# Optimization experiments

Measured on AMD Instinct MI355X. Metric: run time of the kernel, lower is better.

Reference implementation:

```python
import jax, jax.numpy as jnp
import numpy as np

B, LQ, LK, D = 2, 2048, 2048, 1024
H, DK, DV = 16, 64, 64
EPS = 1e-6


def setup_inputs() -> dict:
    key = jax.random.key(0)
    ks = jax.random.split(key, 12)
    s = 1.0 / np.sqrt(D)
    return {
        "PE_states": jax.random.normal(ks[0], (B, LK, D), jnp.float32),
        "global_state": jax.random.normal(ks[1], (B, LQ, D), jnp.float32),
        "PE_statements": jax.random.normal(ks[2], (B, LK, D), jnp.float32),
        "PE_operators": jax.random.normal(ks[3], (B, LK, D), jnp.float32),
        "PE_solution_scores": jax.random.uniform(ks[4], (B, LK), jnp.float32),
        "mask": jax.random.randint(ks[5], (B, LQ, LK), 0, 2, jnp.int32),
        "w_q": jax.random.normal(ks[6], (D, H * DK), jnp.float32) * s,
        "w_k": jax.random.normal(ks[7], (D, H * DK), jnp.float32) * s,
        "w_v": jax.random.normal(ks[8], (D, H * DV), jnp.float32) * s,
        "w_fc": jax.random.normal(ks[9], (H * DV, D), jnp.float32) * s,
        "ln_gamma": jnp.ones((D,), jnp.float32),
        "ln_beta": jnp.zeros((D,), jnp.float32),
    }


def _layer_norm(x, gamma, beta):
    mu = jnp.mean(x, axis=-1, keepdims=True)
    var = jnp.mean(jnp.square(x - mu), axis=-1, keepdims=True)
    return (x - mu) * jax.lax.rsqrt(var + EPS) * gamma + beta


def reference(PE_states, global_state, PE_statements, PE_operators,
              PE_solution_scores, mask, w_q, w_k, w_v, w_fc, ln_gamma, ln_beta):
    # att_type == 'ca_sc', query_mode == 'PE', dropout == 0
    residual = global_state  # [B, LQ, D]
    q = (global_state @ w_q).reshape(B, LQ, H, DK).transpose(0, 2, 1, 3)   # bhqd
    k = (PE_states @ w_k).reshape(B, LK, H, DK).transpose(0, 2, 1, 3)      # bhkd
    v_s = (PE_statements @ w_v).reshape(B, LK, H, DV).transpose(0, 2, 1, 3)
    v_o = (PE_operators @ w_v).reshape(B, LK, H, DV).transpose(0, 2, 1, 3)

    temp = jnp.asarray(DK, jnp.float32) ** 0.5
    attn = jnp.einsum('bhqd,bhkd->bhqk', q / temp, k)  # [B,H,LQ,LK]
    # PE_solution_scores: per-key bias broadcast over heads and queries
    attn = (attn + PE_solution_scores[:, None, None, :]) / 2.0
    attn = jnp.where(mask[:, None, :, :] == 0, jnp.float32(-1e9), attn)
    attn = jax.nn.softmax(attn, axis=-1)

    def head_out(v):
        o = jnp.einsum('bhqk,bhkd->bhqd', attn, v)
        o = o.transpose(0, 2, 1, 3).reshape(B, LQ, H * DV)
        o = o @ w_fc + residual
        return _layer_norm(o, ln_gamma, ln_beta)

    statement_pred = head_out(v_s)
    operator_pred = head_out(v_o)
    return statement_pred, operator_pred
```

## Files before the change

### kernel.cpp

```cpp
#include <hip/hip_runtime.h>


typedef unsigned short u16;
typedef unsigned int   u32;
typedef unsigned long long u64;

typedef __attribute__((ext_vector_type(8))) short frag_ab;
typedef __attribute__((ext_vector_type(4))) float frag_cd;
typedef __attribute__((ext_vector_type(16))) float f32x16;
typedef __attribute__((ext_vector_type(8))) unsigned short u16x8;
typedef __attribute__((ext_vector_type(4))) unsigned short u16x4;
typedef __attribute__((ext_vector_type(2))) unsigned int u32x2;
typedef __attribute__((ext_vector_type(4))) int int4v;

__device__ __forceinline__ u16 f2bf(float f) {
    u32 x = __builtin_bit_cast(u32, f);
    return (u16)((x + 0x7fffu + ((x >> 16) & 1u)) >> 16);
}

__device__ __forceinline__ u32 pkbf(float a, float b) {
    return __builtin_amdgcn_perm(__builtin_bit_cast(u32, b),
                                 __builtin_bit_cast(u32, a), 0x07060302u);
}

#define GLDS16(gsrc, ldst)                                                     \
    __builtin_amdgcn_global_load_lds(                                          \
        (const __attribute__((address_space(1))) void*)(gsrc),                 \
        (__attribute__((address_space(3))) void*)(ldst), 16, 0, 0)

#define MFMA32(a, b, c) __builtin_amdgcn_mfma_f32_32x32x16_bf16(a, b, c, 0, 0, 0)

__global__ __launch_bounds__(256) void downcast_kernel(
    const float* __restrict__ in0, const float* __restrict__ in1,
    const float* __restrict__ in2, const float* __restrict__ in3,
    u16* __restrict__ out)
{
    int z = blockIdx.y;
    const float* in = z == 0 ? in0 : z == 1 ? in1 : z == 2 ? in2 : in3;
    u16* o = out + (size_t)z * 4194304;
    size_t i = ((size_t)blockIdx.x * 256 + threadIdx.x) * 8;
    float4 f0 = *(const float4*)(in + i);
    float4 f1 = *(const float4*)(in + i + 4);
    u16x8 t;
    t[0] = f2bf(f0.x); t[1] = f2bf(f0.y); t[2] = f2bf(f0.z); t[3] = f2bf(f0.w);
    t[4] = f2bf(f1.x); t[5] = f2bf(f1.y); t[6] = f2bf(f1.z); t[7] = f2bf(f1.w);
    *(u16x8*)(o + i) = t;
}

__global__ __launch_bounds__(256) void transpose_kernel(
    const float* __restrict__ w_q, const float* __restrict__ w_k,
    const float* __restrict__ w_v, const float* __restrict__ w_fc,
    u16* __restrict__ wqT, u16* __restrict__ wkT,
    u16* __restrict__ wvT, u16* __restrict__ wfcT)
{
    __shared__ u16 tile[32][33];
    int z = blockIdx.z;
    const float* in = z == 0 ? w_q : z == 1 ? w_k : z == 2 ? w_v : w_fc;
    u16* out = z == 0 ? wqT : z == 1 ? wkT : z == 2 ? wvT : wfcT;
    int bx = blockIdx.x * 32, by = blockIdx.y * 32;
    int tx = threadIdx.x & 31, ty = threadIdx.x >> 5;
    for (int i = 0; i < 32; i += 8)
        tile[ty + i][tx] = f2bf(in[(size_t)(by + ty + i) * 1024 + bx + tx]);
    __syncthreads();
    for (int i = 0; i < 32; i += 8)
        out[(size_t)(bx + ty + i) * 1024 + by + tx] = tile[tx][ty + i];
}

__global__ __launch_bounds__(256) void pack_mask_kernel(
    const int* __restrict__ mask, u64* __restrict__ bits)
{
    long long gid = (long long)blockIdx.x * 256 + threadIdx.x;
    int v = mask[gid];
    u64 bl = __ballot(v != 0);
    if ((threadIdx.x & 63) == 0) bits[gid >> 6] = bl;
}

__device__ __forceinline__ void gemm_core(
    const u16* __restrict__ A, const u16* __restrict__ BT,
    int bm, int bn, u16* Al, u16* Bl, frag_cd acc[4][4])
{
    const int tid = threadIdx.x;
    const int wave = tid >> 6, lane = tid & 63;
    const int ln15 = lane & 15, quad = lane >> 4;
    const int wm4 = (wave & 1) * 4, wn4 = (wave >> 1) * 4;

    for (int k0 = 0; k0 < 1024; k0 += 64) {
        for (int s = 0; s < 4; s++) {
            int f = wave * 4 + s;
            int grp = f >> 1, ks = f & 1;
            size_t col = k0 + ks * 32 + quad * 8;
            GLDS16(&A[(size_t)(bm + grp * 16 + ln15) * 1024 + col], Al + f * 512);
            GLDS16(&BT[(size_t)(bn + grp * 16 + ln15) * 1024 + col], Bl + f * 512);
        }
        __syncthreads();
        for (int ks = 0; ks < 2; ks++) {
            frag_ab a[4], b[4];
            for (int i = 0; i < 4; i++)
                a[i] = *(const frag_ab*)(Al + ((wm4 + i) * 2 + ks) * 512 + lane * 8);
            for (int j = 0; j < 4; j++)
                b[j] = *(const frag_ab*)(Bl + ((wn4 + j) * 2 + ks) * 512 + lane * 8);
            for (int i = 0; i < 4; i++)
                for (int j = 0; j < 4; j++)
                    acc[i][j] = __builtin_amdgcn_mfma_f32_16x16x32_bf16(a[i], b[j], acc[i][j], 0, 0, 0);
        }
        __syncthreads();
    }
}

__global__ __launch_bounds__(256, 3) void proj_gemm_kernel(
    const u16* __restrict__ Ab4,
    const u16* __restrict__ wqT, const u16* __restrict__ wkT, const u16* __restrict__ wvT,
    u16* __restrict__ Qb, u16* __restrict__ Kb,
    u16* __restrict__ VsT_g, u16* __restrict__ VoT_g)
{
    __shared__ alignas(16) u16 Al[16 * 512];
    __shared__ alignas(16) u16 Bl[16 * 512];
    const int z = blockIdx.z;
    const u16* A = Ab4 + (size_t)z * 4194304;
    const u16* BT = z == 0 ? wqT : z == 1 ? wkT : wvT;
    const int bm = blockIdx.x * 128, bn = blockIdx.y * 128;
    frag_cd acc[4][4] = {};
    gemm_core(A, BT, bm, bn, Al, Bl, acc);

    const int lane = threadIdx.x & 63;
    const int wave = threadIdx.x >> 6;
    const int ln15 = lane & 15, quad = lane >> 4;
    const int wm = (wave & 1) * 64, wn = (wave >> 1) * 64;
    if (z < 2) {
        u16* C = z == 0 ? Qb : Kb;
        const float qsc = z == 0 ? 0.09016844f : 1.0f;
        for (int i = 0; i < 4; i++) for (int j = 0; j < 4; j++) {
            int row0 = bm + wm + i * 16 + quad * 4;
            int col = bn + wn + j * 16 + ln15;
            for (int r = 0; r < 4; r++)
                C[(size_t)(row0 + r) * 1024 + col] = f2bf(acc[i][j][r] * qsc);
        }
    } else {
        u16* C = z == 2 ? VsT_g : VoT_g;
        for (int i = 0; i < 4; i++) for (int j = 0; j < 4; j++) {
            int row0 = bm + wm + i * 16 + quad * 4;
            int col = bn + wn + j * 16 + ln15;
            u16x4 t;
            for (int r = 0; r < 4; r++) t[r] = f2bf(acc[i][j][r]);
            *(u16x4*)&C[(size_t)col * 4096 + row0] = t;
        }
    }
}

__global__ __launch_bounds__(256, 3) void fc_gemm_kernel(
    const u16* __restrict__ Osb, const u16* __restrict__ Oob, const u16* __restrict__ wfcT,
    const float* __restrict__ resid, float* __restrict__ preLN)
{
    __shared__ alignas(16) u16 Al[16 * 512];
    __shared__ alignas(16) u16 Bl[16 * 512];
    const int z = blockIdx.z;
    const u16* A = z == 0 ? Osb : Oob;
    float* Cf = preLN + (size_t)z * 4194304;
    const int bm = blockIdx.x * 128, bn = blockIdx.y * 128;
    frag_cd acc[4][4] = {};
    gemm_core(A, wfcT, bm, bn, Al, Bl, acc);

    const int lane = threadIdx.x & 63;
    const int wave = threadIdx.x >> 6;
    const int ln15 = lane & 15, quad = lane >> 4;
    const int wm = (wave & 1) * 64, wn = (wave >> 1) * 64;
    for (int i = 0; i < 4; i++) for (int j = 0; j < 4; j++) {
        int row0 = bm + wm + i * 16 + quad * 4;
        int col = bn + wn + j * 16 + ln15;
        for (int r = 0; r < 4; r++) {
            size_t off = (size_t)(row0 + r) * 1024 + col;
            Cf[off] = acc[i][j][r] + resid[off];
        }
    }
}

__device__ __forceinline__ void flash_stage(
    const u16* __restrict__ Kp, const u16* __restrict__ VsT, const u16* __restrict__ VoT,
    int b, int h, int kt, int wave, int ln31, int hi, u16* buf)
{
    const int k0 = kt * 64;
    for (int s = 0; s < 6; s++) {
        int t = wave * 6 + s;
        const u16* g;
        if (t < 8) {
            int n = t >> 2, ks = t & 3;
            g = &Kp[(size_t)(b * 2048 + k0 + n * 32 + ln31) * 1024 + h * 64 + ks * 16 + hi * 8];
        } else if (t < 16) {
            int dt = (t >> 2) & 1, sk = t & 3;
            g = &VsT[(size_t)(h * 64 + dt * 32 + ln31) * 4096 + b * 2048 + k0 + sk * 16 + hi * 8];
        } else {
            int dt = (t >> 2) & 1, sk = t & 3;
            g = &VoT[(size_t)(h * 64 + dt * 32 + ln31) * 4096 + b * 2048 + k0 + sk * 16 + hi * 8];
        }
        GLDS16(g, buf + t * 512);
    }
}

__global__ __launch_bounds__(256, 2) void flash_kernel(
    const u16* __restrict__ Q, const u16* __restrict__ Kp,
    const u16* __restrict__ VsT_g, const u16* __restrict__ VoT_g,
    const float* __restrict__ scores, const u64* __restrict__ mbits,
    u16* __restrict__ Os, u16* __restrict__ Oo)
{
    __shared__ alignas(16) u16 KV[2][24 * 512];
    const int bid = blockIdx.x;
    const int xcd = bid & 7;
    const int qt = (bid >> 3) & 15;
    const int g = xcd + 8 * (bid >> 7);
    const int h = g & 15, b = g >> 4;
    const int tid = threadIdx.x;
    const int wave = tid >> 6, lane = tid & 63;
    const int ln31 = lane & 31, hi = lane >> 5;
    const int qbase = b * 2048 + qt * 128 + wave * 32;
    const int qrow = qbase + ln31;

    frag_ab aq0, aq1, aq2, aq3;
    {
        const u16* qp = &Q[(size_t)qrow * 1024 + h * 64 + hi * 8];
        aq0 = *(const frag_ab*)(qp);
        aq1 = *(const frag_ab*)(qp + 16);
        aq2 = *(const frag_ab*)(qp + 32);
        aq3 = *(const frag_ab*)(qp + 48);
    }
    frag_ab bbias = {};
    bbias[0] = (short)0x3F80; bbias[1] = (short)0x3F80;

    f32x16 os0 = {}, os1 = {}, oo0 = {}, oo1 = {};
    float l0 = 0.f, l1 = 0.f;
    const int shl4 = 4 - 4 * hi;

    auto softmax16 = [&](f32x16& s, u32 wa, float& lacc) {
#pragma unroll
        for (int r = 0; r < 16; r++) {
            const int bitc = (r & 3) + 8 * (r >> 2);
            u32 m = (u32)(((int)(wa << (27 - bitc))) >> 31);
            float e = __builtin_amdgcn_exp2f(s[r]);
            u32 pb = __builtin_bit_cast(u32, e) & m;
            float pf = __builtin_bit_cast(float, pb);
            lacc += pf;
            s[r] = pf;
        }
    };

    flash_stage(Kp, VsT_g, VoT_g, b, h, 0, wave, ln31, hi, KV[0]);

    for (int kt = 0; kt < 32; kt++) {
        const int p = kt & 1;
        float sc0f = scores[b * 2048 + kt * 64 + ln31];
        float sc1f = scores[b * 2048 + kt * 64 + 32 + ln31];
        u64 w = mbits[(size_t)qrow * 32 + kt];
        __syncthreads();
        if (kt < 31)
            flash_stage(Kp, VsT_g, VoT_g, b, h, kt + 1, wave, ln31, hi, KV[p ^ 1]);
        const u16* bufp = KV[p];

        frag_ab ab0 = {}, ab1 = {};
        if (!hi) {
            float t0 = sc0f * 0.72134752f;
            u16 c0 = f2bf(t0);
            ab0[0] = (short)c0;
            ab0[1] = (short)f2bf(t0 - __builtin_bit_cast(float, (u32)c0 << 16));
            float t1 = sc1f * 0.72134752f;
            u16 c1 = f2bf(t1);
            ab1[0] = (short)c1;
            ab1[1] = (short)f2bf(t1 - __builtin_bit_cast(float, (u32)c1 << 16));
        }

        f32x16 sacc0 = {}, sacc1 = {};
        sacc0 = MFMA32(ab0, bbias, sacc0);
        sacc1 = MFMA32(ab1, bbias, sacc1);
#pragma unroll
        for (int ks = 0; ks < 4; ks++) {
            frag_ab ak0 = *(const frag_ab*)(bufp + (0 * 4 + ks) * 512 + lane * 8);
            frag_ab ak1 = *(const frag_ab*)(bufp + (1 * 4 + ks) * 512 + lane * 8);
            frag_ab q = ks == 0 ? aq0 : ks == 1 ? aq1 : ks == 2 ? aq2 : aq3;
            sacc0 = MFMA32(ak0, q, sacc0);
            sacc1 = MFMA32(ak1, q, sacc1);
        }

        u32 wa0 = ((u32)w) << shl4;
        u32 wa1 = ((u32)(w >> 32)) << shl4;
        softmax16(sacc0, wa0, l0);
        softmax16(sacc1, wa1, l1);

#pragma unroll
        for (int sk = 0; sk < 4; sk++) {
            const f32x16& ps = (sk < 2) ? sacc0 : sacc1;
            const int e0 = (sk & 1) * 8;
            u32 a0 = pkbf(ps[e0 + 0], ps[e0 + 1]);
            u32 a1 = pkbf(ps[e0 + 2], ps[e0 + 3]);
            u32 b0 = pkbf(ps[e0 + 4], ps[e0 + 5]);
            u32 b1 = pkbf(ps[e0 + 6], ps[e0 + 7]);
            u32x2 r0 = __builtin_amdgcn_permlane32_swap(a0, b0, false, false);
            u32x2 r1 = __builtin_amdgcn_permlane32_swap(a1, b1, false, false);
            int4v iv;
            iv[0] = (int)r0[0]; iv[1] = (int)r1[0];
            iv[2] = (int)r0[1]; iv[3] = (int)r1[1];
            frag_ab ap = __builtin_bit_cast(frag_ab, iv);
            frag_ab bs0 = *(const frag_ab*)(bufp + (8 + sk) * 512 + lane * 8);
            frag_ab bs1 = *(const frag_ab*)(bufp + (12 + sk) * 512 + lane * 8);
            frag_ab bo0 = *(const frag_ab*)(bufp + (16 + sk) * 512 + lane * 8);
            frag_ab bo1 = *(const frag_ab*)(bufp + (20 + sk) * 512 + lane * 8);
            os0 = MFMA32(ap, bs0, os0);
            os1 = MFMA32(ap, bs1, os1);
            oo0 = MFMA32(ap, bo0, oo0);
            oo1 = MFMA32(ap, bo1, oo1);
        }
    }

    float l_run = l0 + l1;
    float l_tot = l_run + __shfl_xor(l_run, 32, 64);
#pragma unroll
    for (int r = 0; r < 16; r++) {
        const int qr = (r & 3) + 8 * (r >> 2) + 4 * hi;
        float lv = __shfl(l_tot, qr, 64);
        float inv = 1.0f / fmaxf(lv, 1e-30f);
        size_t row = (size_t)(qbase + qr) * 1024 + h * 64;
        Os[row + ln31]      = f2bf(os0[r] * inv);
        Os[row + 32 + ln31] = f2bf(os1[r] * inv);
        Oo[row + ln31]      = f2bf(oo0[r] * inv);
        Oo[row + 32 + ln31] = f2bf(oo1[r] * inv);
    }
}

__global__ __launch_bounds__(256) void ln_kernel(
    const float* __restrict__ X, const float* __restrict__ gamma, const float* __restrict__ beta,
    float* __restrict__ out)
{
    __shared__ float red[4];
    int row = blockIdx.x;
    int tid = threadIdx.x;
    const float* x = X + (size_t)row * 1024;
    float v[4];
    float s = 0.f;
    for (int i = 0; i < 4; i++) { v[i] = x[tid + i * 256]; s += v[i]; }
    for (int off = 1; off < 64; off <<= 1) s += __shfl_xor(s, off, 64);
    int wv = tid >> 6, ln = tid & 63;
    if (ln == 0) red[wv] = s;
    __syncthreads();
    float mean = (red[0] + red[1] + red[2] + red[3]) * (1.0f / 1024.0f);
    float s2 = 0.f;
    for (int i = 0; i < 4; i++) { float d = v[i] - mean; s2 += d * d; }
    for (int off = 1; off < 64; off <<= 1) s2 += __shfl_xor(s2, off, 64);
    __syncthreads();
    if (ln == 0) red[wv] = s2;
    __syncthreads();
    float var = (red[0] + red[1] + red[2] + red[3]) * (1.0f / 1024.0f);
    float rstd = rsqrtf(var + 1e-6f);
    for (int i = 0; i < 4; i++) {
        int c = tid + i * 256;
        out[(size_t)row * 1024 + c] = (v[i] - mean) * rstd * gamma[c] + beta[c];
    }
}

extern "C" void kernel_launch(void* const* d_in, const int* in_sizes, int n_in,
                              void* d_out, int out_size, void* d_ws, size_t ws_size,
                              hipStream_t stream)
{
    const float* PE_states     = (const float*)d_in[0];
    const float* global_state  = (const float*)d_in[1];
    const float* PE_statements = (const float*)d_in[2];
    const float* PE_operators  = (const float*)d_in[3];
    const float* scores        = (const float*)d_in[4];
    const int*   mask          = (const int*)d_in[5];
    const float* w_q  = (const float*)d_in[6];
    const float* w_k  = (const float*)d_in[7];
    const float* w_v  = (const float*)d_in[8];
    const float* w_fc = (const float*)d_in[9];
    const float* gamma = (const float*)d_in[10];
    const float* beta  = (const float*)d_in[11];
    float* out = (float*)d_out;

    char* ws = (char*)d_ws;
    const size_t MB = 1u << 20;
    u16* Ab4   = (u16*)(ws + 0 * MB);
    u16* Osb   = (u16*)(ws + 0 * MB);
    u16* Oob   = (u16*)(ws + 8 * MB);
    u16* wqT   = (u16*)(ws + 32 * MB);
    u16* wkT   = (u16*)(ws + 34 * MB);
    u16* wvT   = (u16*)(ws + 36 * MB);
    u16* wfcT  = (u16*)(ws + 38 * MB);
    u64* mbits = (u64*)(ws + 40 * MB);
    u16* Qb    = (u16*)(ws + 41 * MB);
    u16* Kb    = (u16*)(ws + 49 * MB);
    u16* VsT_g = (u16*)(ws + 57 * MB);
    u16* VoT_g = (u16*)(ws + 65 * MB);
    float* preLN = (float*)(ws + 41 * MB);

    downcast_kernel<<<dim3(2048, 4), 256, 0, stream>>>(
        global_state, PE_states, PE_statements, PE_operators, Ab4);
    transpose_kernel<<<dim3(32, 32, 4), 256, 0, stream>>>(w_q, w_k, w_v, w_fc, wqT, wkT, wvT, wfcT);
    pack_mask_kernel<<<32768, 256, 0, stream>>>(mask, mbits);

    proj_gemm_kernel<<<dim3(32, 8, 4), 256, 0, stream>>>(
        Ab4, wqT, wkT, wvT, Qb, Kb, VsT_g, VoT_g);

    flash_kernel<<<dim3(512), 256, 0, stream>>>(Qb, Kb, VsT_g, VoT_g, scores, mbits, Osb, Oob);

    fc_gemm_kernel<<<dim3(32, 8, 2), 256, 0, stream>>>(Osb, Oob, wfcT, global_state, preLN);
    ln_kernel<<<8192, 256, 0, stream>>>(preLN, gamma, beta, out);
}
```

Before: 367.7 us.

## Pipeline GEMM K-loop with a 4-slot LDS ring and async prefetch

Replaces the synchronous load-then-compute GEMM loop with a 4-deep shared-memory ring buffer, using k-steps of 32. Each step prefetches three stages ahead via direct global-to-LDS loads, waits with a partial vmcnt and issues one barrier per step instead of two. The goal is to hide global load latency behind MFMA work in the projection and FC GEMMs. LDS per block grows to 64 KB, so the launch-bounds occupancy hint drops from 3 to 2 blocks, and the tail iterations redundantly reload the last stage.

```diff
diff --git a/kernel.cpp b/kernel.cpp
--- a/kernel.cpp
+++ b/kernel.cpp
@@ -77,50 +77,58 @@
 
 __device__ __forceinline__ void gemm_core(
     const u16* __restrict__ A, const u16* __restrict__ BT,
-    int bm, int bn, u16* Al, u16* Bl, frag_cd acc[4][4])
+    int bm, int bn, u16* ring, frag_cd acc[4][4])
 {
     const int tid = threadIdx.x;
     const int wave = tid >> 6, lane = tid & 63;
     const int ln15 = lane & 15, quad = lane >> 4;
     const int wm4 = (wave & 1) * 4, wn4 = (wave >> 1) * 4;
 
-    for (int k0 = 0; k0 < 1024; k0 += 64) {
-        for (int s = 0; s < 4; s++) {
-            int f = wave * 4 + s;
-            int grp = f >> 1, ks = f & 1;
-            size_t col = k0 + ks * 32 + quad * 8;
-            GLDS16(&A[(size_t)(bm + grp * 16 + ln15) * 1024 + col], Al + f * 512);
-            GLDS16(&BT[(size_t)(bn + grp * 16 + ln15) * 1024 + col], Bl + f * 512);
-        }
-        __syncthreads();
-        for (int ks = 0; ks < 2; ks++) {
-            frag_ab a[4], b[4];
-            for (int i = 0; i < 4; i++)
-                a[i] = *(const frag_ab*)(Al + ((wm4 + i) * 2 + ks) * 512 + lane * 8);
+    auto stage = [&](int ts, int slot) {
+        u16* dst = ring + slot * 8192;
+        size_t col = (size_t)ts * 32 + quad * 8;
+        for (int s = 0; s < 2; s++) {
+            int f = wave * 2 + s;
+            GLDS16(&A [(size_t)(bm + f * 16 + ln15) * 1024 + col], dst + f * 512);
+            GLDS16(&BT[(size_t)(bn + f * 16 + ln15) * 1024 + col], dst + 4096 + f * 512);
+        }
+    };
+
+    stage(0, 0); stage(1, 1); stage(2, 2);
+
+    for (int t = 0; t < 32; t++) {
+        asm volatile("s_waitcnt vmcnt(8) lgkmcnt(0)" ::: "memory");
+        __builtin_amdgcn_s_barrier();
+        __builtin_amdgcn_sched_barrier(0);
+        int ts = t + 3 <= 31 ? t + 3 : 31;
+        stage(ts, (t + 3) & 3);
+        __builtin_amdgcn_sched_barrier(0);
+        const u16* buf = ring + (t & 3) * 8192;
+        frag_ab a[4], b[4];
+        for (int i = 0; i < 4; i++)
+            a[i] = *(const frag_ab*)(buf + (wm4 + i) * 512 + lane * 8);
+        for (int j = 0; j < 4; j++)
+            b[j] = *(const frag_ab*)(buf + 4096 + (wn4 + j) * 512 + lane * 8);
+        for (int i = 0; i < 4; i++)
             for (int j = 0; j < 4; j++)
-                b[j] = *(const frag_ab*)(Bl + ((wn4 + j) * 2 + ks) * 512 + lane * 8);
-            for (int i = 0; i < 4; i++)
-                for (int j = 0; j < 4; j++)
-                    acc[i][j] = __builtin_amdgcn_mfma_f32_16x16x32_bf16(a[i], b[j], acc[i][j], 0, 0, 0);
-        }
-        __syncthreads();
-    }
-}
-
-__global__ __launch_bounds__(256, 3) void proj_gemm_kernel(
+                acc[i][j] = __builtin_amdgcn_mfma_f32_16x16x32_bf16(a[i], b[j], acc[i][j], 0, 0, 0);
+    }
+    asm volatile("s_waitcnt vmcnt(0)" ::: "memory");
+}
+
+__global__ __launch_bounds__(256, 2) void proj_gemm_kernel(
     const u16* __restrict__ Ab4,
     const u16* __restrict__ wqT, const u16* __restrict__ wkT, const u16* __restrict__ wvT,
     u16* __restrict__ Qb, u16* __restrict__ Kb,
     u16* __restrict__ VsT_g, u16* __restrict__ VoT_g)
 {
-    __shared__ alignas(16) u16 Al[16 * 512];
-    __shared__ alignas(16) u16 Bl[16 * 512];
+    __shared__ alignas(16) u16 ring[4 * 8192];
     const int z = blockIdx.z;
     const u16* A = Ab4 + (size_t)z * 4194304;
     const u16* BT = z == 0 ? wqT : z == 1 ? wkT : wvT;
     const int bm = blockIdx.x * 128, bn = blockIdx.y * 128;
     frag_cd acc[4][4] = {};
-    gemm_core(A, BT, bm, bn, Al, Bl, acc);
+    gemm_core(A, BT, bm, bn, ring, acc);
 
     const int lane = threadIdx.x & 63;
     const int wave = threadIdx.x >> 6;
@@ -147,18 +155,17 @@
     }
 }
 
-__global__ __launch_bounds__(256, 3) void fc_gemm_kernel(
+__global__ __launch_bounds__(256, 2) void fc_gemm_kernel(
     const u16* __restrict__ Osb, const u16* __restrict__ Oob, const u16* __restrict__ wfcT,
     const float* __restrict__ resid, float* __restrict__ preLN)
 {
-    __shared__ alignas(16) u16 Al[16 * 512];
-    __shared__ alignas(16) u16 Bl[16 * 512];
+    __shared__ alignas(16) u16 ring[4 * 8192];
     const int z = blockIdx.z;
     const u16* A = z == 0 ? Osb : Oob;
     float* Cf = preLN + (size_t)z * 4194304;
     const int bm = blockIdx.x * 128, bn = blockIdx.y * 128;
     frag_cd acc[4][4] = {};
-    gemm_core(A, wfcT, bm, bn, Al, Bl, acc);
+    gemm_core(A, wfcT, bm, bn, ring, acc);
 
     const int lane = threadIdx.x & 63;
     const int wave = threadIdx.x >> 6;
```

After: 369.6 us. Within noise of the previous version (+0.5%).
